# Optimization experiments

Hardware: AMD Instinct MI355X
Metric: run time of the kernel (lower is better)

Reference implementation:

```python
import jax, jax.numpy as jnp
import numpy as np

_EPS = 1e-5

def _block(x, g, b, W, bias):
    # BatchNorm1d (training-mode batch stats, biased variance) -> Linear -> ReLU; Dropout treated as identity (eval)
    m = jnp.mean(x, axis=0)
    v = jnp.mean((x - m) ** 2, axis=0)
    xn = (x - m) * jax.lax.rsqrt(v + _EPS) * g + b
    return jax.nn.relu(xn @ W + bias)

def _seg_mean(h, dst, n):
    # DGL mean reducer: 0 for nodes with no in-edges
    s = jax.ops.segment_sum(h, dst, num_segments=n)
    c = jax.ops.segment_sum(jnp.ones((h.shape[0], 1), h.dtype), dst, num_segments=n)
    return s / jnp.maximum(c, 1.0)

def setup_inputs() -> dict:
    key = jax.random.key(0)
    ks = iter(jax.random.split(key, 64))
    N, E, F, D = 20000, 300000, 128, 128
    d = {}
    d['win_f'] = jax.random.normal(next(ks), (E, F), jnp.float32)
    d['loss_f'] = jax.random.normal(next(ks), (E, F), jnp.float32)
    for name, din, dout in [('wi', F, D), ('li', F, D), ('src', D, D), ('dst', D, D), ('wl', D, D), ('ll', D, D), ('out', 2 * D, D)]:
        d[name + '_g'] = jnp.ones((din,), jnp.float32)
        d[name + '_b'] = jnp.zeros((din,), jnp.float32)
        d[name + '_W'] = jax.random.normal(next(ks), (din, dout), jnp.float32) * 0.05
        d[name + '_bias'] = jnp.zeros((dout,), jnp.float32)
    for name in ['win_src', 'win_dst', 'loss_src', 'loss_dst']:
        d[name] = jax.random.randint(next(ks), (E,), 0, N, jnp.int32)
    d['n_nodes'] = N
    return d

def reference(win_f, loss_f,
              wi_g, wi_b, wi_W, wi_bias,
              li_g, li_b, li_W, li_bias,
              src_g, src_b, src_W, src_bias,
              dst_g, dst_b, dst_W, dst_bias,
              wl_g, wl_b, wl_W, wl_bias,
              ll_g, ll_b, ll_W, ll_bias,
              out_g, out_b, out_W, out_bias,
              win_src, win_dst, loss_src, loss_dst, n_nodes):
    DEPTH = 3
    hw = _block(win_f, wi_g, wi_b, wi_W, wi_bias)   # [Ew, D]
    hl = _block(loss_f, li_g, li_b, li_W, li_bias)  # [El, D]
    # edge_to_node: per-etype scatter-mean, cross-type mean over the 2 etypes
    h = 0.5 * (_seg_mean(hw, win_dst, n_nodes) + _seg_mean(hl, loss_dst, n_nodes))  # [N, D]
    f = h
    for _ in range(DEPTH):
        hu = _block(h, src_g, src_b, src_W, src_bias)
        hv = _block(h, dst_g, dst_b, dst_W, dst_bias)
        hw = hu[win_src] + hv[win_dst]
        hl = hu[loss_src] + hv[loss_dst] # u_add_v on 'loss' edges
        hw = _block(hw, wl_g, wl_b, wl_W, wl_bias)
        hl = _block(hl, ll_g, ll_b, ll_W, ll_bias)
        h = 0.5 * (_seg_mean(hw, win_dst, n_nodes) + _seg_mean(hl, loss_dst, n_nodes))
    return _block(jnp.concatenate([f, h], axis=1), out_g, out_b, out_W, out_bias)
```

## Files before the change

### kernel.cpp

```cpp
#include <hip/hip_runtime.h>

#define NPART_MAX 2048

typedef __attribute__((ext_vector_type(8))) short short8;
typedef __attribute__((ext_vector_type(4))) float f32x4;

__device__ __forceinline__ float bf2f(uint u) {
    union { uint u; float f; } v; v.u = u << 16; return v.f;
}
__device__ __forceinline__ ushort f2bf(float f) {
    union { float f; uint u; } v; v.f = f;
    uint r = v.u + 0x7fffu + ((v.u >> 16) & 1u);
    return (ushort)(r >> 16);
}

__global__ __launch_bounds__(256) void hist2(const int* __restrict__ dw, const int* __restrict__ dl,
                                             int E, int* __restrict__ cw, int* __restrict__ cl) {
    const int half = gridDim.x >> 1;
    const bool second = (int)blockIdx.x >= half;
    const int* dst = second ? dl : dw;
    int* cnt = second ? cl : cw;
    const int b = second ? blockIdx.x - half : blockIdx.x;
    for (int e = b * 256 + threadIdx.x; e < E; e += half * 256)
        atomicAdd(&cnt[dst[e]], 1);
}

__global__ __launch_bounds__(256) void scan2(const int* __restrict__ cw, const int* __restrict__ cl,
                                             int n, int* offw, int* curw, int* offl, int* curl) {
    const int* cnt = blockIdx.x ? cl : cw;
    int* off = blockIdx.x ? offl : offw;
    int* cur = blockIdx.x ? curl : curw;
    __shared__ int warpsums[4];
    __shared__ int s_carry;
    if (threadIdx.x == 0) s_carry = 0;
    __syncthreads();
    for (int base = 0; base < n; base += 1024) {
        int i0 = base + threadIdx.x * 4;
        int v0 = (i0 + 0 < n) ? cnt[i0 + 0] : 0;
        int v1 = (i0 + 1 < n) ? cnt[i0 + 1] : 0;
        int v2 = (i0 + 2 < n) ? cnt[i0 + 2] : 0;
        int v3 = (i0 + 3 < n) ? cnt[i0 + 3] : 0;
        int tsum = v0 + v1 + v2 + v3;
        int lane = threadIdx.x & 63, w = threadIdx.x >> 6;
        int x = tsum;
        for (int d = 1; d < 64; d <<= 1) {
            int y = __shfl_up(x, d);
            if (lane >= d) x += y;
        }
        if (lane == 63) warpsums[w] = x;
        __syncthreads();
        int woff = 0;
        for (int k = 0; k < w; ++k) woff += warpsums[k];
        int excl = x - tsum + woff + s_carry;
        if (i0 + 0 < n) { off[i0 + 0] = excl; cur[i0 + 0] = excl; } excl += v0;
        if (i0 + 1 < n) { off[i0 + 1] = excl; cur[i0 + 1] = excl; } excl += v1;
        if (i0 + 2 < n) { off[i0 + 2] = excl; cur[i0 + 2] = excl; } excl += v2;
        if (i0 + 3 < n) { off[i0 + 3] = excl; cur[i0 + 3] = excl; } excl += v3;
        __syncthreads();
        if (threadIdx.x == 255) s_carry = excl;
        __syncthreads();
    }
    if (threadIdx.x == 0) off[n] = s_carry;
}

__global__ __launch_bounds__(256) void scatter2(
    const int* __restrict__ sw, const int* __restrict__ dw,
    const int* __restrict__ sl, const int* __restrict__ dl, int E,
    int* __restrict__ curw, int* __restrict__ curl,
    int* __restrict__ permw, int* __restrict__ ssrcw, int* __restrict__ sdstw,
    int* __restrict__ perml, int* __restrict__ ssrcl, int* __restrict__ sdstl) {
    const int half = gridDim.x >> 1;
    const bool second = (int)blockIdx.x >= half;
    const int* src = second ? sl : sw;
    const int* dst = second ? dl : dw;
    int* cursor = second ? curl : curw;
    int* perm = second ? perml : permw;
    int* ssrc = second ? ssrcl : ssrcw;
    int* sdst = second ? sdstl : sdstw;
    const int b = second ? blockIdx.x - half : blockIdx.x;
    for (int e = b * 256 + threadIdx.x; e < E; e += half * 256) {
        int d = dst[e];
        int p = atomicAdd(&cursor[d], 1);
        perm[p] = e;
        ssrc[p] = src[e];
        sdst[p] = d;
    }
}

__device__ __forceinline__ void statsf_body(
    int b, int nb, const float4* __restrict__ x4, int M,
    float* __restrict__ psum, float* __restrict__ psq) {
    const int cg = threadIdx.x & 31;
    const int sub = threadIdx.x >> 5;
    float s0=0,s1=0,s2=0,s3=0,q0=0,q1=0,q2=0,q3=0;
    for (int r = b * 8 + sub; r < M; r += nb * 8) {
        float4 v = x4[(size_t)r * 32 + cg];
        s0 += v.x; q0 += v.x * v.x;
        s1 += v.y; q1 += v.y * v.y;
        s2 += v.z; q2 += v.z * v.z;
        s3 += v.w; q3 += v.w * v.w;
    }
    __shared__ float rs[256][4], rq[256][4];
    rs[threadIdx.x][0]=s0; rs[threadIdx.x][1]=s1; rs[threadIdx.x][2]=s2; rs[threadIdx.x][3]=s3;
    rq[threadIdx.x][0]=q0; rq[threadIdx.x][1]=q1; rq[threadIdx.x][2]=q2; rq[threadIdx.x][3]=q3;
    __syncthreads();
    if (sub == 0) {
        #pragma unroll
        for (int k = 1; k < 8; ++k) {
            s0 += rs[k*32+cg][0]; s1 += rs[k*32+cg][1];
            s2 += rs[k*32+cg][2]; s3 += rs[k*32+cg][3];
            q0 += rq[k*32+cg][0]; q1 += rq[k*32+cg][1];
            q2 += rq[k*32+cg][2]; q3 += rq[k*32+cg][3];
        }
        psum[b*128 + cg*4+0] = s0; psq[b*128 + cg*4+0] = q0;
        psum[b*128 + cg*4+1] = s1; psq[b*128 + cg*4+1] = q1;
        psum[b*128 + cg*4+2] = s2; psq[b*128 + cg*4+2] = q2;
        psum[b*128 + cg*4+3] = s3; psq[b*128 + cg*4+3] = q3;
    }
}

__global__ __launch_bounds__(256) void stats_f32_2(
    const float4* xa, float* psa, float* pqa,
    const float4* xb, float* psb, float* pqb, int M) {
    const int half = gridDim.x >> 1;
    const bool second = (int)blockIdx.x >= half;
    statsf_body(second ? blockIdx.x - half : blockIdx.x, half,
                second ? xb : xa, M, second ? psb : psa, second ? pqb : pqa);
}

__global__ __launch_bounds__(256) void gather_stats2(
    const uint2* __restrict__ hu4, const uint2* __restrict__ hv4,
    const int* __restrict__ sw, const int* __restrict__ dw,
    float* __restrict__ psumW, float* __restrict__ psqW,
    const int* __restrict__ sl, const int* __restrict__ dl,
    float* __restrict__ psumL, float* __restrict__ psqL, int E) {
    const int gh = gridDim.x >> 1;
    const bool second = (int)blockIdx.x >= gh;
    const int* sidx = second ? sl : sw;
    const int* didx = second ? dl : dw;
    float* psum = second ? psumL : psumW;
    float* psq  = second ? psqL  : psqW;
    const int b = second ? blockIdx.x - gh : blockIdx.x;

    const int lane = threadIdx.x & 63;
    const int w = threadIdx.x >> 6;
    const int half = lane >> 5;
    const int cg = lane & 31;
    const int gwave = (b * 256 + threadIdx.x) >> 6;
    const int nwave = (gh * 256) >> 6;
    float s0=0,s1=0,s2=0,s3=0,q0=0,q1=0,q2=0,q3=0;
    for (int base = gwave * 64; base < E; base += nwave * 64) {
        int e = base + lane;
        int su = (e < E) ? sidx[e] : 0;
        int dv = (e < E) ? didx[e] : 0;
        int cnt = min(64, E - base);
        int curd = -1;
        float hv0=0,hv1=0,hv2=0,hv3=0;
        float rs0=0,rs1=0,rs2=0,rs3=0,rq0=0,rq1=0,rq2=0,rq3=0,rlen=0;
        auto flush = [&]() {
            if (curd >= 0) {
                s0 += rs0 + rlen*hv0; q0 += rq0 + 2.f*hv0*rs0 + rlen*hv0*hv0;
                s1 += rs1 + rlen*hv1; q1 += rq1 + 2.f*hv1*rs1 + rlen*hv1*hv1;
                s2 += rs2 + rlen*hv2; q2 += rq2 + 2.f*hv2*rs2 + rlen*hv2*hv2;
                s3 += rs3 + rlen*hv3; q3 += rq3 + 2.f*hv3*rs3 + rlen*hv3*hv3;
            }
        };
        #pragma unroll 4
        for (int j = 0; j < 32; ++j) {
            int eidx = 2 * j + half;
            int a = __shfl(su, eidx), dd = __shfl(dv, eidx);
            if (eidx < cnt) {
                if (dd != curd) {
                    flush();
                    curd = dd;
                    uint2 vv = hv4[(size_t)dd * 32 + cg];
                    hv0 = bf2f(vv.x & 0xffffu); hv1 = bf2f(vv.x >> 16);
                    hv2 = bf2f(vv.y & 0xffffu); hv3 = bf2f(vv.y >> 16);
                    rs0=rs1=rs2=rs3=0; rq0=rq1=rq2=rq3=0; rlen=0;
                }
                uint2 uu = hu4[(size_t)a * 32 + cg];
                float u0 = bf2f(uu.x & 0xffffu), u1 = bf2f(uu.x >> 16);
                float u2 = bf2f(uu.y & 0xffffu), u3 = bf2f(uu.y >> 16);
                rs0 += u0; rq0 += u0*u0;
                rs1 += u1; rq1 += u1*u1;
                rs2 += u2; rq2 += u2*u2;
                rs3 += u3; rq3 += u3*u3;
                rlen += 1.f;
            }
        }
        flush();
    }
    __shared__ float redS[8][32][4], redQ[8][32][4];
    const int ri = w * 2 + half;
    redS[ri][cg][0]=s0; redS[ri][cg][1]=s1; redS[ri][cg][2]=s2; redS[ri][cg][3]=s3;
    redQ[ri][cg][0]=q0; redQ[ri][cg][1]=q1; redQ[ri][cg][2]=q2; redQ[ri][cg][3]=q3;
    __syncthreads();
    if (threadIdx.x < 128) {
        int c = threadIdx.x;
        int cgg = c >> 2, k = c & 3;
        float s = 0.f, q = 0.f;
        #pragma unroll
        for (int i = 0; i < 8; ++i) { s += redS[i][cgg][k]; q += redQ[i][cgg][k]; }
        psum[(size_t)b * 128 + c] = s;
        psq [(size_t)b * 128 + c] = q;
    }
}

__device__ __forceinline__ void reduce_body(
    int c, const float* __restrict__ psum, const float* __restrict__ psq,
    int nblk, int C, int M,
    const float* __restrict__ g1, const float* __restrict__ b1,
    float* __restrict__ scale1, float* __restrict__ shift1,
    const float* g2, const float* b2, float* scale2, float* shift2) {
    double s = 0.0, q = 0.0;
    for (int i = threadIdx.x; i < nblk; i += 256) {
        s += (double)psum[(size_t)i * C + c];
        q += (double)psq [(size_t)i * C + c];
    }
    __shared__ double ss[256], qs[256];
    ss[threadIdx.x] = s; qs[threadIdx.x] = q;
    __syncthreads();
    for (int d = 128; d > 0; d >>= 1) {
        if (threadIdx.x < d) {
            ss[threadIdx.x] += ss[threadIdx.x + d];
            qs[threadIdx.x] += qs[threadIdx.x + d];
        }
        __syncthreads();
    }
    if (threadIdx.x == 0) {
        double m = ss[0] / (double)M;
        double v = qs[0] / (double)M - m * m;
        if (v < 0.0) v = 0.0;
        double rs = 1.0 / sqrt(v + 1e-5);
        float mf = (float)m;
        float sc1 = (float)(rs * (double)g1[c]);
        scale1[c] = sc1;
        shift1[c] = b1[c] - mf * sc1;
        if (g2) {
            float sc2 = (float)(rs * (double)g2[c]);
            scale2[c] = sc2;
            shift2[c] = b2[c] - mf * sc2;
        }
    }
}

__global__ __launch_bounds__(256) void reduce_stats(
    const float* psum, const float* psq, int nblk, int C, int M,
    const float* g1, const float* b1, float* scale1, float* shift1,
    const float* g2, const float* b2, float* scale2, float* shift2) {
    reduce_body(blockIdx.x, psum, psq, nblk, C, M, g1, b1, scale1, shift1, g2, b2, scale2, shift2);
}

__global__ __launch_bounds__(256) void reduce_stats2(
    const float* psumA, const float* psqA, int nblkA, int CA, int MA,
    const float* gA, const float* bA, float* scaleA, float* shiftA,
    const float* psumB, const float* psqB, int nblkB, int CB, int MB,
    const float* gB, const float* bB, float* scaleB, float* shiftB) {
    if ((int)blockIdx.x < CA)
        reduce_body(blockIdx.x, psumA, psqA, nblkA, CA, MA, gA, bA, scaleA, shiftA,
                    nullptr, nullptr, nullptr, nullptr);
    else
        reduce_body(blockIdx.x - CA, psumB, psqB, nblkB, CB, MB, gB, bB, scaleB, shiftB,
                    nullptr, nullptr, nullptr, nullptr);
}

__device__ __forceinline__ void fold_body(
    int b, const float* __restrict__ scale, const float* __restrict__ shift, int C,
    const float* __restrict__ W, const float* __restrict__ bias,
    ushort* __restrict__ Wp, float* __restrict__ beff) {
    const int KT = C / 32;
    __shared__ float slab[32 * 128];
    if (b < KT) {
        const int kt = b;
        for (int i = threadIdx.x; i < 32 * 128; i += 256) {
            int kr = i >> 7, d = i & 127;
            int c = kt * 32 + kr;
            slab[i] = W[(size_t)c * 128 + d] * scale[c];
        }
        __syncthreads();
        #pragma unroll
        for (int t0 = 0; t0 < 512; t0 += 256) {
            int t = t0 + threadIdx.x;
            int lane = t & 63, dt = t >> 6;
            int d = dt * 16 + (lane & 15);
            int kb = (lane >> 4) * 8;
            uint4 o;
            o.x = (uint)f2bf(slab[(kb+0)*128 + d]) | ((uint)f2bf(slab[(kb+1)*128 + d]) << 16);
            o.y = (uint)f2bf(slab[(kb+2)*128 + d]) | ((uint)f2bf(slab[(kb+3)*128 + d]) << 16);
            o.z = (uint)f2bf(slab[(kb+4)*128 + d]) | ((uint)f2bf(slab[(kb+5)*128 + d]) << 16);
            o.w = (uint)f2bf(slab[(kb+6)*128 + d]) | ((uint)f2bf(slab[(kb+7)*128 + d]) << 16);
            *(uint4*)(Wp + (size_t)((dt * KT + kt) * 64 + lane) * 8) = o;
        }
    } else {
        const int bb = b - KT;
        const int dl = threadIdx.x & 15, ci = threadIdx.x >> 4;
        const int d = bb * 16 + dl;
        float a = 0.f;
        for (int c = ci; c < C; c += 16)
            a += shift[c] * W[(size_t)c * 128 + d];
        float* red = slab;
        red[threadIdx.x] = a;
        __syncthreads();
        if (ci == 0) {
            #pragma unroll
            for (int k = 1; k < 16; ++k) a += red[k * 16 + dl];
            beff[d] = bias[d] + a;
        }
    }
}

__global__ __launch_bounds__(256) void pack_fold_par(
    const float* scale, const float* shift, int C,
    const float* W, const float* bias, ushort* Wp, float* beff) {
    fold_body(blockIdx.x, scale, shift, C, W, bias, Wp, beff);
}

__global__ __launch_bounds__(256) void pack_fold2(
    const float* scaleA, const float* shiftA, int CA, const float* WA, const float* biasA,
    ushort* WpA, float* beffA,
    const float* scaleB, const float* shiftB, int CB, const float* WB, const float* biasB,
    ushort* WpB, float* beffB) {
    const int nA = CA / 32 + 8;
    const bool second = (int)blockIdx.x >= nA;
    fold_body(second ? blockIdx.x - nA : blockIdx.x,
              second ? scaleB : scaleA, second ? shiftB : shiftA, second ? CB : CA,
              second ? WB : WA, second ? biasB : biasA,
              second ? WpB : WpA, second ? beffB : beffA);
}

template<int KT, int MODE>
__device__ __forceinline__ void gemm_body(
    int b, const ushort* __restrict__ X,
    const ushort* __restrict__ Wp, const float* __restrict__ beff,
    ushort* __restrict__ Yb, float* __restrict__ Yf, int M) {
    constexpr int K = KT * 32;
    const int lane = threadIdx.x & 63;
    const int w = threadIdx.x >> 6;
    const int r0 = b * 128 + w * 32;
    const int rlo = lane & 15, khi = lane >> 4;

    f32x4 acc[2][8];
    #pragma unroll
    for (int rt = 0; rt < 2; ++rt)
        #pragma unroll
        for (int dt = 0; dt < 8; ++dt)
            acc[rt][dt] = (f32x4){0.f, 0.f, 0.f, 0.f};

    int row[2], idx[2];
    bool ok[2];
    #pragma unroll
    for (int rt = 0; rt < 2; ++rt) {
        row[rt] = r0 + rt * 16 + rlo;
        ok[rt] = row[rt] < M;
        idx[rt] = ok[rt] ? row[rt] : 0;
    }

    for (int kt = 0; kt < KT; ++kt) {
        short8 wf[8];
        #pragma unroll
        for (int dt = 0; dt < 8; ++dt)
            wf[dt] = *(const short8*)(Wp + (size_t)((dt * KT + kt) * 64 + lane) * 8);
        #pragma unroll
        for (int rt = 0; rt < 2; ++rt) {
            short8 bv = *(const short8*)(X + (size_t)idx[rt] * K + kt * 32 + khi * 8);
            #pragma unroll
            for (int dt = 0; dt < 8; ++dt)
                acc[rt][dt] = __builtin_amdgcn_mfma_f32_16x16x32_bf16(wf[dt], bv, acc[rt][dt], 0, 0, 0);
        }
    }

    #pragma unroll
    for (int rt = 0; rt < 2; ++rt) {
        if (!ok[rt]) continue;
        #pragma unroll
        for (int dt = 0; dt < 8; ++dt) {
            float v0, v1, v2, v3;
            if constexpr (MODE == 2) {
                v0 = acc[rt][dt][0]; v1 = acc[rt][dt][1];
                v2 = acc[rt][dt][2]; v3 = acc[rt][dt][3];
            } else {
                const float4 bz = *(const float4*)(beff + dt * 16 + khi * 4);
                v0 = fmaxf(acc[rt][dt][0] + bz.x, 0.f);
                v1 = fmaxf(acc[rt][dt][1] + bz.y, 0.f);
                v2 = fmaxf(acc[rt][dt][2] + bz.z, 0.f);
                v3 = fmaxf(acc[rt][dt][3] + bz.w, 0.f);
            }
            if constexpr (MODE == 1) {
                *(float4*)(Yf + (size_t)row[rt] * 128 + dt * 16 + khi * 4) = make_float4(v0, v1, v2, v3);
            } else {
                uint2 pk;
                pk.x = (uint)f2bf(v0) | ((uint)f2bf(v1) << 16);
                pk.y = (uint)f2bf(v2) | ((uint)f2bf(v3) << 16);
                *(uint2*)(Yb + (size_t)row[rt] * 128 + dt * 16 + khi * 4) = pk;
            }
        }
    }
}

__global__ __launch_bounds__(256) void gemm_final(
    const ushort* X, const ushort* Wp, const float* beff, float* Yf, int M) {
    gemm_body<8, 1>(blockIdx.x, X, Wp, beff, nullptr, Yf, M);
}

__global__ __launch_bounds__(256) void gemm_dual(
    const ushort* X,
    const ushort* Wp1, const float* beff1, ushort* Y1,
    const ushort* Wp2, const float* beff2, ushort* Y2, int M) {
    const int half = gridDim.x >> 1;
    const bool second = (int)blockIdx.x >= half;
    gemm_body<4, 0>(second ? blockIdx.x - half : blockIdx.x, X,
                    second ? Wp2 : Wp1, second ? beff2 : beff1,
                    second ? Y2 : Y1, nullptr, M);
}

__global__ __launch_bounds__(256) void gemm_quad(
    const ushort* hu, const ushort* hv,
    const ushort* Wp1, const ushort* Wp2,
    ushort* HUw, ushort* HVw, ushort* HUl, ushort* HVl, int M) {
    const int gq = gridDim.x >> 2;
    const int q = blockIdx.x / gq;
    const int b = blockIdx.x - q * gq;
    const ushort* X = (q & 1) ? hv : hu;
    const ushort* Wp = (q >= 2) ? Wp2 : Wp1;
    ushort* Y = (q == 0) ? HUw : (q == 1) ? HVw : (q == 2) ? HUl : HVl;
    gemm_body<4, 2>(b, X, Wp, nullptr, Y, nullptr, M);
}

__device__ __forceinline__ void gemm_seg_body(
    int b, const float* __restrict__ XF, const int* __restrict__ perm,
    const int* __restrict__ sdst, const int* __restrict__ cnt,
    const ushort* __restrict__ Wp, const float* __restrict__ beff,
    float* __restrict__ hacc, int M) {
    constexpr int KT = 4;
    __shared__ ushort tile[64 * 132];
    __shared__ int   s_node[64];
    __shared__ float s_scale[64];
    const int tid = threadIdx.x;
    const int lane = tid & 63;
    const int w = tid >> 6;
    const int rb = b * 64;
    const int rlo = lane & 15, khi = lane >> 4;

    if (tid < 64) {
        int r = rb + tid;
        int nd = (r < M) ? sdst[r] : -1;
        s_node[tid] = nd;
        s_scale[tid] = (nd >= 0) ? 0.5f / fmaxf((float)cnt[nd], 1.f) : 0.f;
    }

    f32x4 acc[8];
    #pragma unroll
    for (int dt = 0; dt < 8; ++dt)
        acc[dt] = (f32x4){0.f, 0.f, 0.f, 0.f};

    const int row = rb + w * 16 + rlo;
    const bool ok = row < M;
    const int pidx = ok ? perm[row] : 0;

    for (int kt = 0; kt < KT; ++kt) {
        const float* p = XF + (size_t)pidx * 128 + kt * 32 + khi * 8;
        float4 xa = *(const float4*)p;
        float4 xb = *(const float4*)(p + 4);
        short8 bv;
        bv[0] = (short)f2bf(xa.x); bv[1] = (short)f2bf(xa.y);
        bv[2] = (short)f2bf(xa.z); bv[3] = (short)f2bf(xa.w);
        bv[4] = (short)f2bf(xb.x); bv[5] = (short)f2bf(xb.y);
        bv[6] = (short)f2bf(xb.z); bv[7] = (short)f2bf(xb.w);
        #pragma unroll 4
        for (int dt = 0; dt < 8; ++dt) {
            short8 wf = *(const short8*)(Wp + (size_t)((dt * KT + kt) * 64 + lane) * 8);
            acc[dt] = __builtin_amdgcn_mfma_f32_16x16x32_bf16(wf, bv, acc[dt], 0, 0, 0);
        }
    }

    const int rl = w * 16 + rlo;
    #pragma unroll
    for (int dt = 0; dt < 8; ++dt) {
        const float4 bz = *(const float4*)(beff + dt * 16 + khi * 4);
        float v0 = 0.f, v1 = 0.f, v2 = 0.f, v3 = 0.f;
        if (ok) {
            v0 = fmaxf(acc[dt][0] + bz.x, 0.f);
            v1 = fmaxf(acc[dt][1] + bz.y, 0.f);
            v2 = fmaxf(acc[dt][2] + bz.z, 0.f);
            v3 = fmaxf(acc[dt][3] + bz.w, 0.f);
        }
        uint2 pk;
        pk.x = (uint)f2bf(v0) | ((uint)f2bf(v1) << 16);
        pk.y = (uint)f2bf(v2) | ((uint)f2bf(v3) << 16);
        *(uint2*)&tile[rl * 132 + dt * 16 + khi * 4] = pk;
    }
    __syncthreads();

    const int col = tid & 127;
    const int rs = (tid >> 7) * 32;
    int cur = s_node[rs];
    float scl = s_scale[rs];
    float sum = 0.f;
    for (int r = rs; r < rs + 32; ++r) {
        int nd = s_node[r];
        if (nd != cur) {
            if (cur >= 0)
                atomicAdd(&hacc[(size_t)cur * 128 + col], sum * scl);
            cur = nd; scl = s_scale[r]; sum = 0.f;
        }
        sum += bf2f(tile[r * 132 + col]);
    }
    if (cur >= 0)
        atomicAdd(&hacc[(size_t)cur * 128 + col], sum * scl);
}

__global__ __launch_bounds__(256) void gemm_seg2(
    const float* XA, const int* permA, const int* sdstA, const int* cntA,
    const ushort* WpA, const float* beffA, int MA,
    const float* XB, const int* permB, const int* sdstB, const int* cntB,
    const ushort* WpB, const float* beffB, int MB,
    float* hacc) {
    const int half = gridDim.x >> 1;
    const bool second = (int)blockIdx.x >= half;
    gemm_seg_body(second ? blockIdx.x - half : blockIdx.x,
                  second ? XB : XA, second ? permB : permA,
                  second ? sdstB : sdstA, second ? cntB : cntA,
                  second ? WpB : WpA, second ? beffB : beffA,
                  hacc, second ? MB : MA);
}

__global__ __launch_bounds__(256) void edge_seg2(
    const uint* __restrict__ HUw, const uint* __restrict__ HVw,
    const int* __restrict__ sw, const int* __restrict__ dw,
    const int* __restrict__ cw, const float* __restrict__ bw,
    const uint* __restrict__ HUl, const uint* __restrict__ HVl,
    const int* __restrict__ sl, const int* __restrict__ dl,
    const int* __restrict__ cl, const float* __restrict__ bl,
    float* __restrict__ hacc, int E) {
    const int gh = gridDim.x >> 1;
    const bool second = (int)blockIdx.x >= gh;
    const uint* HU = second ? HUl : HUw;
    const uint* HV = second ? HVl : HVw;
    const int* sidx = second ? sl : sw;
    const int* didx = second ? dl : dw;
    const int* cnt = second ? cl : cw;
    const float* beff = second ? bl : bw;
    const int b = second ? blockIdx.x - gh : blockIdx.x;

    const int lane = threadIdx.x & 63;
    const int gwave = (b * 256 + threadIdx.x) >> 6;
    const int nwave = (gh * 256) >> 6;
    const float bz0 = beff[2 * lane];
    const float bz1 = beff[2 * lane + 1];

    for (int base = gwave * 64; base < E; base += nwave * 64) {
        int e = base + lane;
        int su = (e < E) ? sidx[e] : 0;
        int dv = (e < E) ? didx[e] : 0;
        int cn = min(64, E - base);
        int cur = -1; float scl = 0.f, a0 = 0.f, a1 = 0.f, hv0 = 0.f, hv1 = 0.f;
        auto body = [&](int j) {
            int aa = __shfl(su, j), dd = __shfl(dv, j);
            if (dd != cur) {
                if (cur >= 0) {
                    atomicAdd(&hacc[(size_t)cur * 128 + 2 * lane],     a0 * scl);
                    atomicAdd(&hacc[(size_t)cur * 128 + 2 * lane + 1], a1 * scl);
                }
                cur = dd; scl = 0.5f / fmaxf((float)cnt[dd], 1.f); a0 = 0.f; a1 = 0.f;
                uint vv = HV[(size_t)dd * 64 + lane];
                hv0 = bf2f(vv & 0xffffu); hv1 = bf2f(vv >> 16);
            }
            uint uu = HU[(size_t)aa * 64 + lane];
            a0 += fmaxf(bf2f(uu & 0xffffu) + hv0 + bz0, 0.f);
            a1 += fmaxf(bf2f(uu >> 16)     + hv1 + bz1, 0.f);
        };
        if (cn == 64) {
            #pragma unroll 4
            for (int j = 0; j < 64; ++j) body(j);
        } else {
            for (int j = 0; j < cn; ++j) body(j);
        }
        if (cur >= 0) {
            atomicAdd(&hacc[(size_t)cur * 128 + 2 * lane],     a0 * scl);
            atomicAdd(&hacc[(size_t)cur * 128 + 2 * lane + 1], a1 * scl);
        }
    }
}

__global__ __launch_bounds__(256) void finalize_hacc_stats(
    float2* __restrict__ hacc2, uint* __restrict__ h2, uint* __restrict__ fh2,
    int fhsel, int N,
    float* __restrict__ psA, float* __restrict__ pqA, int strideA, int offA,
    float* __restrict__ psB, float* __restrict__ pqB, int strideB, int offB) {
    const int cl = threadIdx.x & 63;
    const int sub = threadIdx.x >> 6;
    float s0=0,s1=0,q0=0,q1=0;
    for (int n = blockIdx.x * 4 + sub; n < N; n += gridDim.x * 4) {
        int i = n * 64 + cl;
        float2 v = hacc2[i];
        uint pk = (uint)f2bf(v.x) | ((uint)f2bf(v.y) << 16);
        h2[i] = pk;
        if (fhsel >= 0) fh2[(size_t)n * 128 + fhsel * 64 + cl] = pk;
        hacc2[i] = make_float2(0.f, 0.f);
        s0 += v.x; q0 += v.x * v.x;
        s1 += v.y; q1 += v.y * v.y;
    }
    __shared__ float red[4][64][4];
    red[sub][cl][0]=s0; red[sub][cl][1]=s1; red[sub][cl][2]=q0; red[sub][cl][3]=q1;
    __syncthreads();
    if (sub == 0) {
        #pragma unroll
        for (int k = 1; k < 4; ++k) {
            s0 += red[k][cl][0]; s1 += red[k][cl][1];
            q0 += red[k][cl][2]; q1 += red[k][cl][3];
        }
        psA[(size_t)blockIdx.x * strideA + offA + 2*cl]     = s0;
        psA[(size_t)blockIdx.x * strideA + offA + 2*cl + 1] = s1;
        pqA[(size_t)blockIdx.x * strideA + offA + 2*cl]     = q0;
        pqA[(size_t)blockIdx.x * strideA + offA + 2*cl + 1] = q1;
        if (psB) {
            psB[(size_t)blockIdx.x * strideB + offB + 2*cl]     = s0;
            psB[(size_t)blockIdx.x * strideB + offB + 2*cl + 1] = s1;
            pqB[(size_t)blockIdx.x * strideB + offB + 2*cl]     = q0;
            pqB[(size_t)blockIdx.x * strideB + offB + 2*cl + 1] = q1;
        }
    }
}

extern "C" void kernel_launch(void* const* d_in, const int* in_sizes, int n_in,
                              void* d_out, int out_size, void* d_ws, size_t ws_size,
                              hipStream_t stream) {
    const float* win_f  = (const float*)d_in[0];
    const float* loss_f = (const float*)d_in[1];
    struct BP { const float *g, *b, *W, *bias; };
    auto bp = [&](int i) { return BP{ (const float*)d_in[i], (const float*)d_in[i+1],
                                      (const float*)d_in[i+2], (const float*)d_in[i+3] }; };
    BP wi = bp(2), li = bp(6), srcp = bp(10), dstp = bp(14), wl = bp(18), ll = bp(22), outp = bp(26);
    const int* win_src  = (const int*)d_in[30];
    const int* win_dst  = (const int*)d_in[31];
    const int* loss_src = (const int*)d_in[32];
    const int* loss_dst = (const int*)d_in[33];
    const int E = in_sizes[30];
    const int N = out_size / 128;
    (void)n_in;

    char* base = (char*)d_ws;
    size_t off_b = 0;
    auto alloc = [&](size_t bytes) {
        size_t cur = off_b;
        off_b += (bytes + 255) & ~(size_t)255;
        return (void*)(base + cur);
    };
    float*  hacc = (float*)alloc((size_t)N * 128 * 4);
    ushort* h    = (ushort*)alloc((size_t)N * 128 * 2);
    ushort* hu   = (ushort*)alloc((size_t)N * 128 * 2);
    ushort* hv   = (ushort*)alloc((size_t)N * 128 * 2);
    ushort* fh   = (ushort*)alloc((size_t)N * 256 * 2);
    ushort* HUw  = (ushort*)alloc((size_t)N * 128 * 2);
    ushort* HVw  = (ushort*)alloc((size_t)N * 128 * 2);
    ushort* HUl  = (ushort*)alloc((size_t)N * 128 * 2);
    ushort* HVl  = (ushort*)alloc((size_t)N * 128 * 2);
    int* cntw  = (int*)alloc((size_t)N * 4);
    int* cntl  = (int*)alloc((size_t)N * 4);
    int* offw  = (int*)alloc((size_t)(N + 1) * 4);
    int* offl  = (int*)alloc((size_t)(N + 1) * 4);
    int* curw  = (int*)alloc((size_t)N * 4);
    int* curl  = (int*)alloc((size_t)N * 4);
    int* permw = (int*)alloc((size_t)E * 4);
    int* ssrcw = (int*)alloc((size_t)E * 4);
    int* sdstw = (int*)alloc((size_t)E * 4);
    int* perml = (int*)alloc((size_t)E * 4);
    int* ssrcl = (int*)alloc((size_t)E * 4);
    int* sdstl = (int*)alloc((size_t)E * 4);
    float* psumW = (float*)alloc((size_t)NPART_MAX * 128 * 4);
    float* psqW  = (float*)alloc((size_t)NPART_MAX * 128 * 4);
    float* psumL = (float*)alloc((size_t)NPART_MAX * 128 * 4);
    float* psqL  = (float*)alloc((size_t)NPART_MAX * 128 * 4);
    float* psumN = (float*)alloc((size_t)512 * 128 * 4);
    float* psqN  = (float*)alloc((size_t)512 * 128 * 4);
    float* psum256 = (float*)alloc((size_t)512 * 256 * 4);
    float* psq256  = (float*)alloc((size_t)512 * 256 * 4);
    float* scal1 = (float*)alloc(256 * 4);
    float* shif1 = (float*)alloc(256 * 4);
    float* scal2 = (float*)alloc(256 * 4);
    float* shif2 = (float*)alloc(256 * 4);
    ushort* Wp1 = (ushort*)alloc((size_t)256 * 128 * 2);
    ushort* Wp2 = (ushort*)alloc((size_t)256 * 128 * 2);
    float* beff1 = (float*)alloc(128 * 4);
    float* beff2 = (float*)alloc(128 * 4);
    if (off_b > ws_size) return;

    const int gE64 = (E + 63) / 64;
    const int gN = (N + 127) / 128;
    const int NBF = 1024;
    const int NBG = 2048;
    const int NBN = 512;

    hipMemsetAsync(cntw, 0, (size_t)N * 4, stream);
    hipMemsetAsync(cntl, 0, (size_t)N * 4, stream);
    hipMemsetAsync(hacc, 0, (size_t)N * 128 * 4, stream);
    hist2<<<2048, 256, 0, stream>>>(win_dst, loss_dst, E, cntw, cntl);
    scan2<<<2, 256, 0, stream>>>(cntw, cntl, N, offw, curw, offl, curl);
    scatter2<<<2048, 256, 0, stream>>>(win_src, win_dst, loss_src, loss_dst, E,
                                       curw, curl, permw, ssrcw, sdstw, perml, ssrcl, sdstl);

    stats_f32_2<<<2 * NBF, 256, 0, stream>>>(
        (const float4*)win_f, psumW, psqW,
        (const float4*)loss_f, psumL, psqL, E);
    reduce_stats2<<<256, 256, 0, stream>>>(
        psumW, psqW, NBF, 128, E, wi.g, wi.b, scal1, shif1,
        psumL, psqL, NBF, 128, E, li.g, li.b, scal2, shif2);
    pack_fold2<<<24, 256, 0, stream>>>(scal1, shif1, 128, wi.W, wi.bias, Wp1, beff1,
                                       scal2, shif2, 128, li.W, li.bias, Wp2, beff2);
    gemm_seg2<<<2 * gE64, 256, 0, stream>>>(
        win_f, permw, sdstw, cntw, Wp1, beff1, E,
        loss_f, perml, sdstl, cntl, Wp2, beff2, E, hacc);
    finalize_hacc_stats<<<NBN, 256, 0, stream>>>(
        (float2*)hacc, (uint*)h, (uint*)fh, 0, N,
        psumN, psqN, 128, 0, psum256, psq256, 256, 0);

    for (int it = 0; it < 3; ++it) {
        reduce_stats<<<128, 256, 0, stream>>>(psumN, psqN, NBN, 128, N, srcp.g, srcp.b, scal1, shif1,
                                              dstp.g, dstp.b, scal2, shif2);
        pack_fold2<<<24, 256, 0, stream>>>(scal1, shif1, 128, srcp.W, srcp.bias, Wp1, beff1,
                                           scal2, shif2, 128, dstp.W, dstp.bias, Wp2, beff2);
        gemm_dual<<<2 * gN, 256, 0, stream>>>(h, Wp1, beff1, hu, Wp2, beff2, hv, N);

        gather_stats2<<<2 * NBG, 256, 0, stream>>>(
            (const uint2*)hu, (const uint2*)hv,
            ssrcw, sdstw, psumW, psqW, ssrcl, sdstl, psumL, psqL, E);
        reduce_stats2<<<256, 256, 0, stream>>>(
            psumW, psqW, NBG, 128, E, wl.g, wl.b, scal1, shif1,
            psumL, psqL, NBG, 128, E, ll.g, ll.b, scal2, shif2);
        pack_fold2<<<24, 256, 0, stream>>>(scal1, shif1, 128, wl.W, wl.bias, Wp1, beff1,
                                           scal2, shif2, 128, ll.W, ll.bias, Wp2, beff2);
        gemm_quad<<<4 * gN, 256, 0, stream>>>(hu, hv, Wp1, Wp2, HUw, HVw, HUl, HVl, N);
        edge_seg2<<<2 * NBG, 256, 0, stream>>>(
            (const uint*)HUw, (const uint*)HVw, ssrcw, sdstw, cntw, beff1,
            (const uint*)HUl, (const uint*)HVl, ssrcl, sdstl, cntl, beff2,
            hacc, E);
        if (it < 2) {
            finalize_hacc_stats<<<NBN, 256, 0, stream>>>(
                (float2*)hacc, (uint*)h, (uint*)fh, -1, N,
                psumN, psqN, 128, 0, nullptr, nullptr, 0, 0);
        } else {
            finalize_hacc_stats<<<NBN, 256, 0, stream>>>(
                (float2*)hacc, (uint*)h, (uint*)fh, 1, N,
                psum256, psq256, 256, 128, nullptr, nullptr, 0, 0);
        }
    }

    reduce_stats<<<256, 256, 0, stream>>>(psum256, psq256, NBN, 256, N, outp.g, outp.b, scal1, shif1,
                                          nullptr, nullptr, nullptr, nullptr);
    pack_fold_par<<<16, 256, 0, stream>>>(scal1, shif1, 256, outp.W, outp.bias, Wp1, beff1);
    gemm_final<<<gN, 256, 0, stream>>>(fh, Wp1, beff1, (float*)d_out, N);
}
```

Before: 810.3 us.

## Emit bf16 copies of edge features during stats pass and widen per-lane edge accumulation

The stats pass over the fp32 edge features now also writes a bf16 copy of each input, when workspace allows. The first segmented GEMM then gathers permuted rows from that half-size buffer instead of re-reading and converting fp32. The edge scatter kernel now has each lane handle four columns, with the two half-waves taking alternate edges, and the segment flush in gemm_seg reads pairs of bf16 values. The trade is an extra 2×E×128×2 bytes of writes and workspace in exchange for fewer bytes on the random gather, along with fewer shuffle iterations per edge.

```diff
diff --git a/kernel.cpp b/kernel.cpp
--- a/kernel.cpp
+++ b/kernel.cpp
@@ -88,13 +88,19 @@
 }
 
 __device__ __forceinline__ void statsf_body(
-    int b, int nb, const float4* __restrict__ x4, int M,
+    int b, int nb, const float4* __restrict__ x4, int M, uint2* __restrict__ xb2,
     float* __restrict__ psum, float* __restrict__ psq) {
     const int cg = threadIdx.x & 31;
     const int sub = threadIdx.x >> 5;
     float s0=0,s1=0,s2=0,s3=0,q0=0,q1=0,q2=0,q3=0;
     for (int r = b * 8 + sub; r < M; r += nb * 8) {
         float4 v = x4[(size_t)r * 32 + cg];
+        if (xb2) {
+            uint2 o;
+            o.x = (uint)f2bf(v.x) | ((uint)f2bf(v.y) << 16);
+            o.y = (uint)f2bf(v.z) | ((uint)f2bf(v.w) << 16);
+            xb2[(size_t)r * 32 + cg] = o;
+        }
         s0 += v.x; q0 += v.x * v.x;
         s1 += v.y; q1 += v.y * v.y;
         s2 += v.z; q2 += v.z * v.z;
@@ -119,13 +125,14 @@
     }
 }
 
-__global__ __launch_bounds__(256) void stats_f32_2(
-    const float4* xa, float* psa, float* pqa,
-    const float4* xb, float* psb, float* pqb, int M) {
+__global__ __launch_bounds__(256) void stats_conv2(
+    const float4* xa, uint2* xba, float* psa, float* pqa,
+    const float4* xb, uint2* xbb, float* psb, float* pqb, int M) {
     const int half = gridDim.x >> 1;
     const bool second = (int)blockIdx.x >= half;
     statsf_body(second ? blockIdx.x - half : blockIdx.x, half,
-                second ? xb : xa, M, second ? psb : psa, second ? pqb : pqa);
+                second ? xb : xa, M, second ? xbb : xba,
+                second ? psb : psa, second ? pqb : pqa);
 }
 
 __global__ __launch_bounds__(256) void gather_stats2(
@@ -426,8 +433,9 @@
     gemm_body<4, 2>(b, X, Wp, nullptr, Y, nullptr, M);
 }
 
+template<bool BF>
 __device__ __forceinline__ void gemm_seg_body(
-    int b, const float* __restrict__ XF, const int* __restrict__ perm,
+    int b, const void* __restrict__ Xv, const int* __restrict__ perm,
     const int* __restrict__ sdst, const int* __restrict__ cnt,
     const ushort* __restrict__ Wp, const float* __restrict__ beff,
     float* __restrict__ hacc, int M) {
@@ -458,14 +466,18 @@
     const int pidx = ok ? perm[row] : 0;
 
     for (int kt = 0; kt < KT; ++kt) {
-        const float* p = XF + (size_t)pidx * 128 + kt * 32 + khi * 8;
-        float4 xa = *(const float4*)p;
-        float4 xb = *(const float4*)(p + 4);
         short8 bv;
-        bv[0] = (short)f2bf(xa.x); bv[1] = (short)f2bf(xa.y);
-        bv[2] = (short)f2bf(xa.z); bv[3] = (short)f2bf(xa.w);
-        bv[4] = (short)f2bf(xb.x); bv[5] = (short)f2bf(xb.y);
-        bv[6] = (short)f2bf(xb.z); bv[7] = (short)f2bf(xb.w);
+        if constexpr (BF) {
+            bv = *(const short8*)((const ushort*)Xv + (size_t)pidx * 128 + kt * 32 + khi * 8);
+        } else {
+            const float* p = (const float*)Xv + (size_t)pidx * 128 + kt * 32 + khi * 8;
+            float4 xa = *(const float4*)p;
+            float4 xb = *(const float4*)(p + 4);
+            bv[0] = (short)f2bf(xa.x); bv[1] = (short)f2bf(xa.y);
+            bv[2] = (short)f2bf(xa.z); bv[3] = (short)f2bf(xa.w);
+            bv[4] = (short)f2bf(xb.x); bv[5] = (short)f2bf(xb.y);
+            bv[6] = (short)f2bf(xb.z); bv[7] = (short)f2bf(xb.w);
+        }
         #pragma unroll 4
         for (int dt = 0; dt < 8; ++dt) {
             short8 wf = *(const short8*)(Wp + (size_t)((dt * KT + kt) * 64 + lane) * 8);
@@ -491,51 +503,58 @@
     }
     __syncthreads();
 
-    const int col = tid & 127;
-    const int rs = (tid >> 7) * 32;
+    const int cp = tid & 63;
+    const int rs = (tid >> 6) * 16;
     int cur = s_node[rs];
     float scl = s_scale[rs];
-    float sum = 0.f;
-    for (int r = rs; r < rs + 32; ++r) {
+    float su0 = 0.f, su1 = 0.f;
+    for (int r = rs; r < rs + 16; ++r) {
         int nd = s_node[r];
         if (nd != cur) {
-            if (cur >= 0)
-                atomicAdd(&hacc[(size_t)cur * 128 + col], sum * scl);
-            cur = nd; scl = s_scale[r]; sum = 0.f;
-        }
-        sum += bf2f(tile[r * 132 + col]);
-    }
-    if (cur >= 0)
-        atomicAdd(&hacc[(size_t)cur * 128 + col], sum * scl);
-}
-
+            if (cur >= 0) {
+                atomicAdd(&hacc[(size_t)cur * 128 + 2*cp],     su0 * scl);
+                atomicAdd(&hacc[(size_t)cur * 128 + 2*cp + 1], su1 * scl);
+            }
+            cur = nd; scl = s_scale[r]; su0 = 0.f; su1 = 0.f;
+        }
+        uint u = *(const uint*)&tile[r * 132 + 2*cp];
+        su0 += bf2f(u & 0xffffu);
+        su1 += bf2f(u >> 16);
+    }
+    if (cur >= 0) {
+        atomicAdd(&hacc[(size_t)cur * 128 + 2*cp],     su0 * scl);
+        atomicAdd(&hacc[(size_t)cur * 128 + 2*cp + 1], su1 * scl);
+    }
+}
+
+template<bool BF>
 __global__ __launch_bounds__(256) void gemm_seg2(
-    const float* XA, const int* permA, const int* sdstA, const int* cntA,
+    const void* XA, const int* permA, const int* sdstA, const int* cntA,
     const ushort* WpA, const float* beffA, int MA,
-    const float* XB, const int* permB, const int* sdstB, const int* cntB,
+    const void* XB, const int* permB, const int* sdstB, const int* cntB,
     const ushort* WpB, const float* beffB, int MB,
     float* hacc) {
     const int half = gridDim.x >> 1;
     const bool second = (int)blockIdx.x >= half;
-    gemm_seg_body(second ? blockIdx.x - half : blockIdx.x,
-                  second ? XB : XA, second ? permB : permA,
-                  second ? sdstB : sdstA, second ? cntB : cntA,
-                  second ? WpB : WpA, second ? beffB : beffA,
-                  hacc, second ? MB : MA);
+    gemm_seg_body<BF>(second ? blockIdx.x - half : blockIdx.x,
+                      second ? XB : XA, second ? permB : permA,
+                      second ? sdstB : sdstA, second ? cntB : cntA,
+                      second ? WpB : WpA, second ? beffB : beffA,
+                      hacc, second ? MB : MA);
 }
 
 __global__ __launch_bounds__(256) void edge_seg2(
-    const uint* __restrict__ HUw, const uint* __restrict__ HVw,
+    const uint2* __restrict__ HUw, const uint2* __restrict__ HVw,
     const int* __restrict__ sw, const int* __restrict__ dw,
     const int* __restrict__ cw, const float* __restrict__ bw,
-    const uint* __restrict__ HUl, const uint* __restrict__ HVl,
+    const uint2* __restrict__ HUl, const uint2* __restrict__ HVl,
     const int* __restrict__ sl, const int* __restrict__ dl,
     const int* __restrict__ cl, const float* __restrict__ bl,
     float* __restrict__ hacc, int E) {
     const int gh = gridDim.x >> 1;
     const bool second = (int)blockIdx.x >= gh;
-    const uint* HU = second ? HUl : HUw;
-    const uint* HV = second ? HVl : HVw;
+    const uint2* HU = second ? HUl : HUw;
+    const uint2* HV = second ? HVl : HVw;
     const int* sidx = second ? sl : sw;
     const int* didx = second ? dl : dw;
     const int* cnt = second ? cl : cw;
@@ -543,42 +562,51 @@
     const int b = second ? blockIdx.x - gh : blockIdx.x;
 
     const int lane = threadIdx.x & 63;
+    const int half = lane >> 5;
+    const int cg = lane & 31;
     const int gwave = (b * 256 + threadIdx.x) >> 6;
     const int nwave = (gh * 256) >> 6;
-    const float bz0 = beff[2 * lane];
-    const float bz1 = beff[2 * lane + 1];
+    const float4 bz = *(const float4*)(beff + 4 * cg);
 
     for (int base = gwave * 64; base < E; base += nwave * 64) {
         int e = base + lane;
         int su = (e < E) ? sidx[e] : 0;
         int dv = (e < E) ? didx[e] : 0;
         int cn = min(64, E - base);
-        int cur = -1; float scl = 0.f, a0 = 0.f, a1 = 0.f, hv0 = 0.f, hv1 = 0.f;
-        auto body = [&](int j) {
-            int aa = __shfl(su, j), dd = __shfl(dv, j);
-            if (dd != cur) {
-                if (cur >= 0) {
-                    atomicAdd(&hacc[(size_t)cur * 128 + 2 * lane],     a0 * scl);
-                    atomicAdd(&hacc[(size_t)cur * 128 + 2 * lane + 1], a1 * scl);
+        int cur = -1;
+        float scl = 0.f;
+        float a0 = 0.f, a1 = 0.f, a2 = 0.f, a3 = 0.f;
+        float hv0 = 0.f, hv1 = 0.f, hv2 = 0.f, hv3 = 0.f;
+        auto flushA = [&]() {
+            if (cur >= 0) {
+                float* p = &hacc[(size_t)cur * 128 + 4 * cg];
+                atomicAdd(p + 0, a0 * scl);
+                atomicAdd(p + 1, a1 * scl);
+                atomicAdd(p + 2, a2 * scl);
+                atomicAdd(p + 3, a3 * scl);
+            }
+        };
+        #pragma unroll 4
+        for (int j = 0; j < 32; ++j) {
+            int eidx = 2 * j + half;
+            int aa = __shfl(su, eidx), dd = __shfl(dv, eidx);
+            if (eidx < cn) {
+                if (dd != cur) {
+                    flushA();
+                    cur = dd; scl = 0.5f / fmaxf((float)cnt[dd], 1.f);
+                    a0 = a1 = a2 = a3 = 0.f;
+                    uint2 vv = HV[(size_t)dd * 32 + cg];
+                    hv0 = bf2f(vv.x & 0xffffu); hv1 = bf2f(vv.x >> 16);
+                    hv2 = bf2f(vv.y & 0xffffu); hv3 = bf2f(vv.y >> 16);
                 }
-                cur = dd; scl = 0.5f / fmaxf((float)cnt[dd], 1.f); a0 = 0.f; a1 = 0.f;
-                uint vv = HV[(size_t)dd * 64 + lane];
-                hv0 = bf2f(vv & 0xffffu); hv1 = bf2f(vv >> 16);
+                uint2 uu = HU[(size_t)aa * 32 + cg];
+                a0 += fmaxf(bf2f(uu.x & 0xffffu) + hv0 + bz.x, 0.f);
+                a1 += fmaxf(bf2f(uu.x >> 16)     + hv1 + bz.y, 0.f);
+                a2 += fmaxf(bf2f(uu.y & 0xffffu) + hv2 + bz.z, 0.f);
+                a3 += fmaxf(bf2f(uu.y >> 16)     + hv3 + bz.w, 0.f);
             }
-            uint uu = HU[(size_t)aa * 64 + lane];
-            a0 += fmaxf(bf2f(uu & 0xffffu) + hv0 + bz0, 0.f);
-            a1 += fmaxf(bf2f(uu >> 16)     + hv1 + bz1, 0.f);
-        };
-        if (cn == 64) {
-            #pragma unroll 4
-            for (int j = 0; j < 64; ++j) body(j);
-        } else {
-            for (int j = 0; j < cn; ++j) body(j);
-        }
-        if (cur >= 0) {
-            atomicAdd(&hacc[(size_t)cur * 128 + 2 * lane],     a0 * scl);
-            atomicAdd(&hacc[(size_t)cur * 128 + 2 * lane + 1], a1 * scl);
-        }
+        }
+        flushA();
     }
 }
 
@@ -684,6 +712,11 @@
     float* beff1 = (float*)alloc(128 * 4);
     float* beff2 = (float*)alloc(128 * 4);
     if (off_b > ws_size) return;
+    size_t off_base = off_b;
+    ushort* Xbf1 = (ushort*)alloc((size_t)E * 128 * 2);
+    ushort* Xbf2 = (ushort*)alloc((size_t)E * 128 * 2);
+    const bool have_x2 = (off_b <= ws_size);
+    if (!have_x2) off_b = off_base;
 
     const int gE64 = (E + 63) / 64;
     const int gN = (N + 127) / 128;
@@ -699,17 +732,23 @@
     scatter2<<<2048, 256, 0, stream>>>(win_src, win_dst, loss_src, loss_dst, E,
                                        curw, curl, permw, ssrcw, sdstw, perml, ssrcl, sdstl);
 
-    stats_f32_2<<<2 * NBF, 256, 0, stream>>>(
-        (const float4*)win_f, psumW, psqW,
-        (const float4*)loss_f, psumL, psqL, E);
+    stats_conv2<<<2 * NBF, 256, 0, stream>>>(
+        (const float4*)win_f,  have_x2 ? (uint2*)Xbf1 : nullptr, psumW, psqW,
+        (const float4*)loss_f, have_x2 ? (uint2*)Xbf2 : nullptr, psumL, psqL, E);
     reduce_stats2<<<256, 256, 0, stream>>>(
         psumW, psqW, NBF, 128, E, wi.g, wi.b, scal1, shif1,
         psumL, psqL, NBF, 128, E, li.g, li.b, scal2, shif2);
     pack_fold2<<<24, 256, 0, stream>>>(scal1, shif1, 128, wi.W, wi.bias, Wp1, beff1,
                                        scal2, shif2, 128, li.W, li.bias, Wp2, beff2);
-    gemm_seg2<<<2 * gE64, 256, 0, stream>>>(
-        win_f, permw, sdstw, cntw, Wp1, beff1, E,
-        loss_f, perml, sdstl, cntl, Wp2, beff2, E, hacc);
+    if (have_x2) {
+        gemm_seg2<true><<<2 * gE64, 256, 0, stream>>>(
+            Xbf1, permw, sdstw, cntw, Wp1, beff1, E,
+            Xbf2, perml, sdstl, cntl, Wp2, beff2, E, hacc);
+    } else {
+        gemm_seg2<false><<<2 * gE64, 256, 0, stream>>>(
+            win_f, permw, sdstw, cntw, Wp1, beff1, E,
+            loss_f, perml, sdstl, cntl, Wp2, beff2, E, hacc);
+    }
     finalize_hacc_stats<<<NBN, 256, 0, stream>>>(
         (float2*)hacc, (uint*)h, (uint*)fh, 0, N,
         psumN, psqN, 128, 0, psum256, psq256, 256, 0);
@@ -731,8 +770,8 @@
                                            scal2, shif2, 128, ll.W, ll.bias, Wp2, beff2);
         gemm_quad<<<4 * gN, 256, 0, stream>>>(hu, hv, Wp1, Wp2, HUw, HVw, HUl, HVl, N);
         edge_seg2<<<2 * NBG, 256, 0, stream>>>(
-            (const uint*)HUw, (const uint*)HVw, ssrcw, sdstw, cntw, beff1,
-            (const uint*)HUl, (const uint*)HVl, ssrcl, sdstl, cntl, beff2,
+            (const uint2*)HUw, (const uint2*)HVw, ssrcw, sdstw, cntw, beff1,
+            (const uint2*)HUl, (const uint2*)HVl, ssrcl, sdstl, cntl, beff2,
             hacc, E);
         if (it < 2) {
             finalize_hacc_stats<<<NBN, 256, 0, stream>>>(
```

Result: slower. 1.191 ms (+47.0%).
